# Kernel tuning notes

Measured on AMD Instinct MI355X. Metric: run time of the kernel, lower is better.

Reference implementation:

```python
import jax, jax.numpy as jnp
import numpy as np
from jax import lax

WIN = 7  # hard-coded winsize in PSF.forward
EPS = 1e-8


def _box_sum(x, n):
    # Sliding n x n window sum with zero padding (== ZeroPad2d(n//2) + unfold sum),
    return lax.reduce_window(x, 0.0, lax.add, (1, 1, n, n), (1, 1, 1, 1), 'SAME')


def _patch_stats(x, n):
    n2 = n * n
    s = _box_sum(x, n)
    s2 = _box_sum(x * x, n)
    mean = s / n2
    # torch .var() default is unbiased (divide by N-1)
    var = (s2 - n2 * mean * mean) / (n2 - 1)
    return mean, jnp.maximum(var, 0.0)


def patch_mv_norm(x, n):
    mean, var = _patch_stats(x, n)
    return (x - mean) / (jnp.sqrt(var) + EPS)


def patch_adain(x, y, n):
    x_norm = patch_mv_norm(x, n)
    y_mean, y_var = _patch_stats(y, n)
    return x_norm * jnp.sqrt(y_var) + y_mean  # note: no eps on y_std, as in source


def conv1x1(x, w, b):
    # x: (B,C,H,W), w: (O,C), b: (O,)
    return jnp.einsum('oc,bchw->bohw', w, x) + b[None, :, None, None]


def setup_inputs() -> dict:
    key = jax.random.key(0)
    ks = jax.random.split(key, 12)
    B, C, H, W = 8, 256, 128, 128
    front = jax.random.normal(ks[0], (B, C, H, W), dtype=jnp.float32)
    back = jax.random.normal(ks[1], (B, C, H, W), dtype=jnp.float32)
    mask = jax.random.uniform(ks[2], (B, 1, H, W), dtype=jnp.float32)
    scale = 0.02
    we = jax.random.normal(ks[3], (C, C), dtype=jnp.float32) * scale
    wf = jax.random.normal(ks[4], (C, C), dtype=jnp.float32) * scale
    wg = jax.random.normal(ks[5], (C, C), dtype=jnp.float32) * scale
    wh = jax.random.normal(ks[6], (C, C), dtype=jnp.float32) * scale
    be = jax.random.normal(ks[7], (C,), dtype=jnp.float32) * scale
    bf = jax.random.normal(ks[8], (C,), dtype=jnp.float32) * scale
    bg = jax.random.normal(ks[9], (C,), dtype=jnp.float32) * scale
    bh = jax.random.normal(ks[10], (C,), dtype=jnp.float32) * scale
    return {'front': front, 'back': back, 'mask': mask,
            'we': we, 'be': be, 'wf': wf, 'bf': bf,
            'wg': wg, 'bg': bg, 'wh': wh, 'bh': bh}


def reference(front, back, mask, we, be, wf, bf, wg, bg, wh, bh):
    b, c, h, w = front.shape
    EE = conv1x1(patch_adain(front, back, WIN), we, be)
    FF = conv1x1(patch_mv_norm(front, WIN), wf, bf)
    GG = conv1x1(patch_mv_norm(back, WIN), wg, bg)
    HH = conv1x1(back, wh, bh)
    # channel-wise cosine similarity between FF and GG
    F_n = jnp.sqrt(jnp.sum(FF * FF, axis=1))  # (B,H,W)
    G_n = jnp.sqrt(jnp.sum(GG * GG, axis=1))
    S = jnp.sum(FF * GG, axis=1) / (F_n * G_n)
    # per-sample spatial min-max normalization
    S_flat = S.reshape(b, h * w)
    s_min = jnp.min(S_flat, axis=1, keepdims=True)
    s_max = jnp.max(S_flat, axis=1, keepdims=True)
    S_n = ((S_flat - s_min) / (s_max - s_min)).reshape(b, 1, h, w)
    fused = S_n * EE + (1.0 - S_n) * HH
    return fused
```

## Files before the change

kernel.cpp:

```cpp
#include <hip/hip_runtime.h>
#include <math.h>

#define PIX 16384
#define TSZ ((size_t)33554432)

typedef __attribute__((ext_vector_type(8))) short  short8;
typedef __attribute__((ext_vector_type(4))) float  float4v;
typedef __attribute__((ext_vector_type(4))) unsigned int uint4v;
typedef __attribute__((ext_vector_type(2))) unsigned int uint2v;

__device__ __forceinline__ unsigned short f2bf(float x) {
  unsigned int u = __float_as_uint(x);
  u += 0x7fffu + ((u >> 16) & 1u);
  return (unsigned short)(u >> 16);
}
__device__ __forceinline__ float bf2f(unsigned short h) {
  return __uint_as_float(((unsigned int)h) << 16);
}
__device__ __forceinline__ unsigned int pack_bf2(float lo, float hi) {
  unsigned int ul = __float_as_uint(lo); ul += 0x7fffu + ((ul >> 16) & 1u);
  unsigned int uh = __float_as_uint(hi); uh += 0x7fffu + ((uh >> 16) & 1u);
  return __builtin_amdgcn_perm(uh, ul, 0x07060302u);
}

#define SB0   __builtin_amdgcn_sched_barrier(0)
#define BARR  __builtin_amdgcn_s_barrier()
#define LGKM0 asm volatile("s_waitcnt lgkmcnt(0)" ::: "memory")
#define VMC(n) asm volatile("s_waitcnt vmcnt(" #n ")" ::: "memory")

__global__ __launch_bounds__(256) void k_prep(const float* __restrict__ we,
                                              const float* __restrict__ wf,
                                              const float* __restrict__ wg,
                                              const float* __restrict__ wh,
                                              unsigned short* __restrict__ wbf) {
  int idx = blockIdx.x * 256 + threadIdx.x;
  int g = idx >> 16, within = idx & 65535;
  const float* src = (g == 0) ? wf : (g == 1) ? wg : (g == 2) ? we : wh;
  int e    = within & 7;
  int lane = (within >> 3) & 63;
  int im   = (within >> 9) & 3;
  int wv   = (within >> 11) & 3;
  int i    = within >> 13;
  int col = lane & 15, q = lane >> 4;
  int m = wv * 64 + im * 16 + col;
  int k = i * 32 + q * 8 + e;
  wbf[idx] = f2bf(src[m * 256 + k]);
}

__global__ __launch_bounds__(256, 4) void k_stats(const float* __restrict__ front,
                                                  const float* __restrict__ back,
                                                  unsigned short* __restrict__ xcm) {
  int blk = blockIdx.x;
  int s   = blk & 7;
  int c   = (blk >> 3) & 255;
  int b   = blk >> 11;
  int t   = threadIdx.x;
  int r0  = s * 16;

  __shared__ float2 vspD[16 * 137];

  size_t planeOff = ((size_t)(b * 256 + c)) * PIX;

  float meanR[8], sdR[8];

  #pragma unroll 1
  for (int phase = 0; phase < 2; ++phase) {
    const float* src = (phase == 0 ? back : front) + planeOff;
    {
      int col = t & 127;
      int rg  = (t >> 7) * 8;
      const float* colp = src + col;
      float xv[14];
      #pragma unroll
      for (int j = 0; j < 14; ++j) {
        int g = r0 + rg - 3 + j;
        float v = 0.f;
        if (g >= 0 && g < 128) v = colp[g * 128];
        xv[j] = v;
      }
      float sm = 0.f, s2 = 0.f;
      #pragma unroll
      for (int j = 0; j < 7; ++j) { sm += xv[j]; s2 = fmaf(xv[j], xv[j], s2); }
      vspD[rg * 137 + col + 3] = make_float2(sm, s2);
      #pragma unroll
      for (int o = 1; o < 8; ++o) {
        float vn = xv[o + 6], vo = xv[o - 1];
        sm += vn - vo;
        s2 += vn * vn - vo * vo;
        vspD[(rg + o) * 137 + col + 3] = make_float2(sm, s2);
      }
      if (t < 96) {
        int rr = t & 15;
        int pc = t >> 4;
        int ac = (pc < 3) ? pc : 128 + pc;
        vspD[rr * 137 + ac] = make_float2(0.f, 0.f);
      }
    }
    LGKM0; BARR;
    {
      int r  = t & 15;
      int c0 = (t >> 4) * 8;
      float2 w[14];
      #pragma unroll
      for (int i = 0; i < 14; ++i) w[i] = vspD[r * 137 + c0 + i];
      float4v x0 = *(const float4v*)(src + (r0 + r) * 128 + c0);
      float4v x1 = *(const float4v*)(src + (r0 + r) * 128 + c0 + 4);
      float xc[8] = {x0[0], x0[1], x0[2], x0[3], x1[0], x1[1], x1[2], x1[3]};
      float sm = 0.f, s2 = 0.f;
      #pragma unroll
      for (int i = 0; i < 7; ++i) { sm += w[i].x; s2 += w[i].y; }
      float nrmv[8], hv[8];
      #pragma unroll
      for (int o = 0; o < 8; ++o) {
        float mean = sm * (1.f / 49.f);
        float var  = (s2 - sm * mean) * (1.f / 48.f);
        var = var > 0.f ? var : 0.f;
        float sd = __builtin_amdgcn_sqrtf(var);
        float x  = xc[o];
        float nrm = (x - mean) * __builtin_amdgcn_rcpf(sd + 1e-8f);
        if (phase == 0) { meanR[o] = mean; sdR[o] = sd; hv[o] = x; }
        else            { hv[o] = nrm * sdR[o] + meanR[o]; }
        nrmv[o] = nrm;
        if (o < 7) { sm += w[o + 7].x - w[o].x; s2 += w[o + 7].y - w[o].y; }
      }
      uint4v nv  = (uint4v){pack_bf2(nrmv[0], nrmv[1]), pack_bf2(nrmv[2], nrmv[3]),
                            pack_bf2(nrmv[4], nrmv[5]), pack_bf2(nrmv[6], nrmv[7])};
      uint4v hvv = (uint4v){pack_bf2(hv[0], hv[1]), pack_bf2(hv[2], hv[3]),
                            pack_bf2(hv[4], hv[5]), pack_bf2(hv[6], hv[7])};
      int p = (r0 + r) * 128 + c0;
      size_t gb2 = (((size_t)(b * 256 + (p >> 6))) * 256 + c) * 64 + (p & 63);
      int tn0 = (phase == 0) ? 1 : 0;
      int tn1 = (phase == 0) ? 3 : 2;
      *(uint4v*)(xcm + (size_t)tn0 * TSZ + gb2) = nv;
      *(uint4v*)(xcm + (size_t)tn1 * TSZ + gb2) = hvv;
    }
    LGKM0; BARR;
  }
}

__device__ __forceinline__ void stage_tile(const unsigned short* __restrict__ Xt,
                                           int k0, int t,
                                           unsigned short* dst) {
  int kk = ((t >> 5) << 2) + ((t & 7) >> 1);
  int px = (((t >> 3) & 3) << 4) + ((t & 1) << 3);
  const unsigned short* src = Xt + (size_t)(k0 << 6) + (kk << 6) + px;
  typedef const __attribute__((address_space(1))) unsigned int GUI;
  typedef __attribute__((address_space(3))) unsigned int LUI;
  __builtin_amdgcn_global_load_lds((GUI*)(unsigned long long)src,
                                   (LUI*)(unsigned)(unsigned long long)(dst + t * 8),
                                   16, 0, 0);
}

#define LOADA(S, I) {                                           \
  af[S][0] = *(const short8*)(Wr + (I) * 8192 + 0 * 512);       \
  af[S][1] = *(const short8*)(Wr + (I) * 8192 + 1 * 512);       \
  af[S][2] = *(const short8*)(Wr + (I) * 8192 + 2 * 512);       \
  af[S][3] = *(const short8*)(Wr + (I) * 8192 + 3 * 512); }

#define TR8(O0,O1,O2,O3,O4,O5,O6,O7)                                              \
  asm volatile("ds_read_b64_tr_b16 %0, %1 offset:" #O0 : "=v"(r0) : "v"(tra));    \
  asm volatile("ds_read_b64_tr_b16 %0, %1 offset:" #O1 : "=v"(r1) : "v"(tra));    \
  asm volatile("ds_read_b64_tr_b16 %0, %1 offset:" #O2 : "=v"(r2) : "v"(tra));    \
  asm volatile("ds_read_b64_tr_b16 %0, %1 offset:" #O3 : "=v"(r3) : "v"(tra));    \
  asm volatile("ds_read_b64_tr_b16 %0, %1 offset:" #O4 : "=v"(r4) : "v"(tra));    \
  asm volatile("ds_read_b64_tr_b16 %0, %1 offset:" #O5 : "=v"(r5) : "v"(tra));    \
  asm volatile("ds_read_b64_tr_b16 %0, %1 offset:" #O6 : "=v"(r6) : "v"(tra));    \
  asm volatile("ds_read_b64_tr_b16 %0, %1 offset:" #O7 : "=v"(r7) : "v"(tra));

#define DOMFMA(MS) {                                                        \
  union BU { unsigned u[4]; short8 s; } bu0, bu1, bu2, bu3;                 \
  bu0.u[0]=r0[0]; bu0.u[1]=r0[1]; bu0.u[2]=r1[0]; bu0.u[3]=r1[1];           \
  bu1.u[0]=r2[0]; bu1.u[1]=r2[1]; bu1.u[2]=r3[0]; bu1.u[3]=r3[1];           \
  bu2.u[0]=r4[0]; bu2.u[1]=r4[1]; bu2.u[2]=r5[0]; bu2.u[3]=r5[1];           \
  bu3.u[0]=r6[0]; bu3.u[1]=r6[1]; bu3.u[2]=r7[0]; bu3.u[3]=r7[1];           \
  short8 bv0 = bu0.s, bv1 = bu1.s, bv2 = bu2.s, bv3 = bu3.s;                \
  _Pragma("unroll")                                                         \
  for (int im = 0; im < 4; ++im) {                                          \
    acc[0][im] = __builtin_amdgcn_mfma_f32_16x16x32_bf16(af[MS][im], bv0, acc[0][im], 0, 0, 0); \
    acc[1][im] = __builtin_amdgcn_mfma_f32_16x16x32_bf16(af[MS][im], bv1, acc[1][im], 0, 0, 0); \
    acc[2][im] = __builtin_amdgcn_mfma_f32_16x16x32_bf16(af[MS][im], bv2, acc[2][im], 0, 0, 0); \
    acc[3][im] = __builtin_amdgcn_mfma_f32_16x16x32_bf16(af[MS][im], bv3, acc[3][im], 0, 0, 0); \
  } }

#define GSTEP(VN, DOSTAGE, K0, SLOT, DOA, AS, AI, MS, O0,O1,O2,O3,O4,O5,O6,O7) \
  SB0;                                                                          \
  if (DOSTAGE) stage_tile(X, K0, t, xt + (SLOT) * 2048);                        \
  SB0;                                                                          \
  if (DOA) LOADA(AS, AI);                                                       \
  SB0;                                                                          \
  VMC(VN);                                                                      \
  SB0; BARR; SB0;                                                               \
  TR8(O0,O1,O2,O3,O4,O5,O6,O7);                                                 \
  LGKM0; SB0;                                                                   \
  DOMFMA(MS);

__device__ __forceinline__ void gemm_pipe(const unsigned short* __restrict__ X,
                                          const unsigned short* __restrict__ Wm,
                                          unsigned short* xt, unsigned xbase,
                                          int mbase, int lane, int t,
                                          float4v acc[4][4]) {
  unsigned tra = xbase + (unsigned)((((lane >> 4)) << 10) + ((lane & 15) << 3));
  const unsigned short* __restrict__ Wr = Wm + ((mbase >> 6) << 11) + lane * 8;

  short8 af[2][4];
  uint2v r0, r1, r2, r3, r4, r5, r6, r7;

  #pragma unroll
  for (int in = 0; in < 4; ++in)
    #pragma unroll
    for (int im = 0; im < 4; ++im)
      acc[in][im] = (float4v){0.f, 0.f, 0.f, 0.f};

  SB0; BARR; SB0;
  stage_tile(X,  0, t, xt + 0 * 2048);
  stage_tile(X, 32, t, xt + 1 * 2048);
  stage_tile(X, 64, t, xt + 2 * 2048);
  SB0;
  LOADA(0, 0);
  SB0;

  GSTEP( 5,  1,  96,  3,   1, 1, 1, 0,      0,  512,  128,  640,  256,  768,  384,  896)
  GSTEP( 5,  1, 128,  4,   1, 0, 2, 1,   4096, 4608, 4224, 4736, 4352, 4864, 4480, 4992)
  GSTEP( 5,  1, 160,  0,   1, 1, 3, 0,   8192, 8704, 8320, 8832, 8448, 8960, 8576, 9088)
  GSTEP( 5,  1, 192,  1,   1, 0, 4, 1,  12288,12800,12416,12928,12544,13056,12672,13184)
  GSTEP( 5,  1, 224,  2,   1, 1, 5, 0,  16384,16896,16512,17024,16640,17152,16768,17280)
  GSTEP( 4,  0,   0,  0,   1, 0, 6, 1,      0,  512,  128,  640,  256,  768,  384,  896)
  GSTEP( 4,  0,   0,  0,   1, 1, 7, 0,   4096, 4608, 4224, 4736, 4352, 4864, 4480, 4992)
  GSTEP( 0,  0,   0,  0,   0, 0, 0, 1,   8192, 8704, 8320, 8832, 8448, 8960, 8576, 9088)
}

__global__ __launch_bounds__(256, 3) void k_gemm1(const unsigned short* __restrict__ xcm,
                                                  const unsigned short* __restrict__ wbf,
                                                  const float* __restrict__ bFF,
                                                  const float* __restrict__ bGG,
                                                  float* __restrict__ Sout) {
  int blk  = blockIdx.x;
  int b    = blk >> 8;
  int pt   = blk & 255;
  int p0   = pt * 64;
  int t    = threadIdx.x;
  int wv   = t >> 6;
  int lane = t & 63;
  int q    = lane >> 4;
  int mbase = wv * 64;

  __shared__ __align__(16) unsigned short xt[5][2048];
  __shared__ float sred[3 * 64];
  if (t < 192) sred[t] = 0.f;
  __syncthreads();
  unsigned xbase = (unsigned)(unsigned long long)&xt[0][0];

  const unsigned short* Xt = xcm + (((size_t)(b * 256 + pt)) << 14);

  float4v aF[4][4], aG[4][4];

  gemm_pipe(Xt + 0 * TSZ, wbf + 0 * 65536, &xt[0][0], xbase, mbase, lane, t, aF);
  gemm_pipe(Xt + 1 * TSZ, wbf + 1 * 65536, &xt[0][0], xbase, mbase, lane, t, aG);
  #pragma unroll
  for (int im = 0; im < 4; ++im) {
    float4v bvF = *(const float4v*)(bFF + mbase + im * 16 + q * 4);
    float4v bvG = *(const float4v*)(bGG + mbase + im * 16 + q * 4);
    #pragma unroll
    for (int in = 0; in < 4; ++in) { aF[in][im] += bvF; aG[in][im] += bvG; }
  }
  #pragma unroll
  for (int in = 0; in < 4; ++in) {
    float d = 0.f, nf = 0.f, ng = 0.f;
    #pragma unroll
    for (int im = 0; im < 4; ++im)
      #pragma unroll
      for (int r = 0; r < 4; ++r) {
        float f = aF[in][im][r], g = aG[in][im][r];
        d += f * g; nf += f * f; ng += g * g;
      }
    d  += __shfl_xor(d, 16);  d  += __shfl_xor(d, 32);
    nf += __shfl_xor(nf, 16); nf += __shfl_xor(nf, 32);
    ng += __shfl_xor(ng, 16); ng += __shfl_xor(ng, 32);
    if (lane < 16) {
      atomicAdd(&sred[0 * 64 + in * 16 + lane], d);
      atomicAdd(&sred[1 * 64 + in * 16 + lane], nf);
      atomicAdd(&sred[2 * 64 + in * 16 + lane], ng);
    }
  }
  __syncthreads();
  if (t < 64) {
    float d = sred[t], nf = sred[64 + t], ng = sred[128 + t];
    Sout[(size_t)b * PIX + p0 + t] = d / (sqrtf(nf) * sqrtf(ng));
  }
}

__global__ __launch_bounds__(256, 3) void k_gemm2(const unsigned short* __restrict__ xcm,
                                                  const unsigned short* __restrict__ wbf,
                                                  const float* __restrict__ bEE,
                                                  const float* __restrict__ bHH,
                                                  const float* __restrict__ S,
                                                  const float* __restrict__ mm,
                                                  float* __restrict__ out) {
  int blk  = blockIdx.x;
  int b    = blk >> 8;
  int pt   = blk & 255;
  int p0   = pt * 64;
  int t    = threadIdx.x;
  int wv   = t >> 6;
  int lane = t & 63;
  int col  = lane & 15;
  int q    = lane >> 4;
  int mbase = wv * 64;

  __shared__ __align__(16) unsigned short xt[5][2048];
  unsigned xbase = (unsigned)(unsigned long long)&xt[0][0];

  const unsigned short* Xt = xcm + (((size_t)(b * 256 + pt)) << 14);

  float4v aE[4][4], aH[4][4];

  gemm_pipe(Xt + 2 * TSZ, wbf + 2 * 65536, &xt[0][0], xbase, mbase, lane, t, aE);
  gemm_pipe(Xt + 3 * TSZ, wbf + 3 * 65536, &xt[0][0], xbase, mbase, lane, t, aH);

  float mn = mm[b * 2], mx = mm[b * 2 + 1];
  float inv = 1.f / (mx - mn);
  float sn[4];
  #pragma unroll
  for (int in = 0; in < 4; ++in)
    sn[in] = (S[(size_t)b * PIX + p0 + in * 16 + col] - mn) * inv;

  #pragma unroll
  for (int im = 0; im < 4; ++im) {
    float4v bvE = *(const float4v*)(bEE + mbase + im * 16 + q * 4);
    float4v bvH = *(const float4v*)(bHH + mbase + im * 16 + q * 4);
    #pragma unroll
    for (int in = 0; in < 4; ++in)
      #pragma unroll
      for (int r = 0; r < 4; ++r) {
        int m = mbase + im * 16 + q * 4 + r;
        float e = aE[in][im][r] + bvE[r];
        float h = aH[in][im][r] + bvH[r];
        out[((size_t)(b * 256 + m)) * PIX + p0 + in * 16 + col] = h + sn[in] * (e - h);
      }
  }
}

__global__ __launch_bounds__(256) void k_minmax(const float* __restrict__ S,
                                                float* __restrict__ mm) {
  int b = blockIdx.x, t = threadIdx.x;
  const float* sp = S + (size_t)b * PIX;
  float mn = 3.0e38f, mx = -3.0e38f;
  for (int i = t; i < PIX; i += 256) { float v = sp[i]; mn = fminf(mn, v); mx = fmaxf(mx, v); }
  #pragma unroll
  for (int o = 32; o >= 1; o >>= 1) {
    mn = fminf(mn, __shfl_xor(mn, o));
    mx = fmaxf(mx, __shfl_xor(mx, o));
  }
  __shared__ float smn[4], smx[4];
  if ((t & 63) == 0) { smn[t >> 6] = mn; smx[t >> 6] = mx; }
  __syncthreads();
  if (t == 0) {
    mn = fminf(fminf(smn[0], smn[1]), fminf(smn[2], smn[3]));
    mx = fmaxf(fmaxf(smx[0], smx[1]), fmaxf(smx[2], smx[3]));
    mm[b * 2] = mn; mm[b * 2 + 1] = mx;
  }
}

extern "C" void kernel_launch(void* const* d_in, const int* in_sizes, int n_in,
                              void* d_out, int out_size, void* d_ws, size_t ws_size,
                              hipStream_t stream) {
  const float* front = (const float*)d_in[0];
  const float* back  = (const float*)d_in[1];
  const float* we = (const float*)d_in[3];
  const float* be = (const float*)d_in[4];
  const float* wf = (const float*)d_in[5];
  const float* bf = (const float*)d_in[6];
  const float* wg = (const float*)d_in[7];
  const float* bg = (const float*)d_in[8];
  const float* wh = (const float*)d_in[9];
  const float* bh = (const float*)d_in[10];

  char* ws = (char*)d_ws;
  unsigned short* xcm  = (unsigned short*)(ws);
  unsigned short* wbf  = (unsigned short*)(ws + 268435456);
  float*          S    = (float*)(ws + 268959744);
  float*          mm   = (float*)(ws + 269484032);
  float*          out  = (float*)d_out;

  k_prep  <<<1024,  256, 0, stream>>>(we, wf, wg, wh, wbf);
  k_stats <<<16384, 256, 0, stream>>>(front, back, xcm);
  k_gemm1 <<<2048,  256, 0, stream>>>(xcm, wbf, bf, bg, S);
  k_minmax<<<8,     256, 0, stream>>>(S, mm);
  k_gemm2 <<<2048,  256, 0, stream>>>(xcm, wbf, be, bh, S, mm, out);
}
```

Measured before the change: 542.7 us.

## Interleave paired GEMMs with deep LDS staging and fuse min-max via atomics

The two back-to-back GEMM pipelines in each kernel are merged into one interleaved pipeline that stages larger chunks of both operand tiles into a 64 KB LDS buffer and alternates MFMA work between the two accumulators. The separate min-max kernel is removed; gemm1 instead reduces each tile's similarity and updates per-batch min/max with atomics on order-preserving uint keys, initialised in the prep kernel. The aim is fewer barriers and pipeline prologues plus one fewer launch. In exchange, occupancy drops from 3 to 2 blocks per CU, and the tile-sized atomics add a small cost.

Measured after the change: 517.3 us. 1.05x faster.

```diff
diff --git a/kernel.cpp b/kernel.cpp
--- a/kernel.cpp
+++ b/kernel.cpp
@@ -23,6 +23,15 @@
   return __builtin_amdgcn_perm(uh, ul, 0x07060302u);
 }
 
+__device__ __forceinline__ unsigned int fkey(float f) {
+  unsigned int u = __float_as_uint(f);
+  return (u & 0x80000000u) ? ~u : (u | 0x80000000u);
+}
+__device__ __forceinline__ float funkey(unsigned int k) {
+  unsigned int u = (k & 0x80000000u) ? (k ^ 0x80000000u) : ~k;
+  return __uint_as_float(u);
+}
+
 #define SB0   __builtin_amdgcn_sched_barrier(0)
 #define BARR  __builtin_amdgcn_s_barrier()
 #define LGKM0 asm volatile("s_waitcnt lgkmcnt(0)" ::: "memory")
@@ -32,7 +41,10 @@
                                               const float* __restrict__ wf,
                                               const float* __restrict__ wg,
                                               const float* __restrict__ wh,
-                                              unsigned short* __restrict__ wbf) {
+                                              unsigned short* __restrict__ wbf,
+                                              unsigned int* __restrict__ mmu) {
+  if (blockIdx.x == 0 && threadIdx.x < 16)
+    mmu[threadIdx.x] = (threadIdx.x & 1) ? 0u : 0xFFFFFFFFu;
   int idx = blockIdx.x * 256 + threadIdx.x;
   int g = idx >> 16, within = idx & 65535;
   const float* src = (g == 0) ? wf : (g == 1) ? wg : (g == 2) ? we : wh;
@@ -151,11 +163,11 @@
                                    16, 0, 0);
 }
 
-#define LOADA(S, I) {                                           \
-  af[S][0] = *(const short8*)(Wr + (I) * 8192 + 0 * 512);       \
-  af[S][1] = *(const short8*)(Wr + (I) * 8192 + 1 * 512);       \
-  af[S][2] = *(const short8*)(Wr + (I) * 8192 + 2 * 512);       \
-  af[S][3] = *(const short8*)(Wr + (I) * 8192 + 3 * 512); }
+#define LOADA(WP, S, I) {                                       \
+  af[S][0] = *(const short8*)(WP + (I) * 8192 + 0 * 512);       \
+  af[S][1] = *(const short8*)(WP + (I) * 8192 + 1 * 512);       \
+  af[S][2] = *(const short8*)(WP + (I) * 8192 + 2 * 512);       \
+  af[S][3] = *(const short8*)(WP + (I) * 8192 + 3 * 512); }
 
 #define TR8(O0,O1,O2,O3,O4,O5,O6,O7)                                              \
   asm volatile("ds_read_b64_tr_b16 %0, %1 offset:" #O0 : "=v"(r0) : "v"(tra));    \
@@ -167,7 +179,7 @@
   asm volatile("ds_read_b64_tr_b16 %0, %1 offset:" #O6 : "=v"(r6) : "v"(tra));    \
   asm volatile("ds_read_b64_tr_b16 %0, %1 offset:" #O7 : "=v"(r7) : "v"(tra));
 
-#define DOMFMA(MS) {                                                        \
+#define DOMFMA(ACC, MS) {                                                   \
   union BU { unsigned u[4]; short8 s; } bu0, bu1, bu2, bu3;                 \
   bu0.u[0]=r0[0]; bu0.u[1]=r0[1]; bu0.u[2]=r1[0]; bu0.u[3]=r1[1];           \
   bu1.u[0]=r2[0]; bu1.u[1]=r2[1]; bu1.u[2]=r3[0]; bu1.u[3]=r3[1];           \
@@ -176,31 +188,29 @@
   short8 bv0 = bu0.s, bv1 = bu1.s, bv2 = bu2.s, bv3 = bu3.s;                \
   _Pragma("unroll")                                                         \
   for (int im = 0; im < 4; ++im) {                                          \
-    acc[0][im] = __builtin_amdgcn_mfma_f32_16x16x32_bf16(af[MS][im], bv0, acc[0][im], 0, 0, 0); \
-    acc[1][im] = __builtin_amdgcn_mfma_f32_16x16x32_bf16(af[MS][im], bv1, acc[1][im], 0, 0, 0); \
-    acc[2][im] = __builtin_amdgcn_mfma_f32_16x16x32_bf16(af[MS][im], bv2, acc[2][im], 0, 0, 0); \
-    acc[3][im] = __builtin_amdgcn_mfma_f32_16x16x32_bf16(af[MS][im], bv3, acc[3][im], 0, 0, 0); \
+    ACC[0][im] = __builtin_amdgcn_mfma_f32_16x16x32_bf16(af[MS][im], bv0, ACC[0][im], 0, 0, 0); \
+    ACC[1][im] = __builtin_amdgcn_mfma_f32_16x16x32_bf16(af[MS][im], bv1, ACC[1][im], 0, 0, 0); \
+    ACC[2][im] = __builtin_amdgcn_mfma_f32_16x16x32_bf16(af[MS][im], bv2, ACC[2][im], 0, 0, 0); \
+    ACC[3][im] = __builtin_amdgcn_mfma_f32_16x16x32_bf16(af[MS][im], bv3, ACC[3][im], 0, 0, 0); \
   } }
 
-#define GSTEP(VN, DOSTAGE, K0, SLOT, DOA, AS, AI, MS, O0,O1,O2,O3,O4,O5,O6,O7) \
-  SB0;                                                                          \
-  if (DOSTAGE) stage_tile(X, K0, t, xt + (SLOT) * 2048);                        \
-  SB0;                                                                          \
-  if (DOA) LOADA(AS, AI);                                                       \
-  SB0;                                                                          \
-  VMC(VN);                                                                      \
-  SB0; BARR; SB0;                                                               \
-  TR8(O0,O1,O2,O3,O4,O5,O6,O7);                                                 \
-  LGKM0; SB0;                                                                   \
-  DOMFMA(MS);
-
-__device__ __forceinline__ void gemm_pipe(const unsigned short* __restrict__ X,
-                                          const unsigned short* __restrict__ Wm,
-                                          unsigned short* xt, unsigned xbase,
-                                          int mbase, int lane, int t,
-                                          float4v acc[4][4]) {
+#define FHALF(OA0,OA1,OA2,OA3,OA4,OA5,OA6,OA7, OB0,OB1,OB2,OB3,OB4,OB5,OB6,OB7)   \
+  TR8(OA0,OA1,OA2,OA3,OA4,OA5,OA6,OA7); LGKM0; SB0; DOMFMA(accF, 0);              \
+  TR8(OB0,OB1,OB2,OB3,OB4,OB5,OB6,OB7); LGKM0; SB0; DOMFMA(accF, 1);
+#define GHALF(OA0,OA1,OA2,OA3,OA4,OA5,OA6,OA7, OB0,OB1,OB2,OB3,OB4,OB5,OB6,OB7)   \
+  TR8(OA0,OA1,OA2,OA3,OA4,OA5,OA6,OA7); LGKM0; SB0; DOMFMA(accG, 0);              \
+  TR8(OB0,OB1,OB2,OB3,OB4,OB5,OB6,OB7); LGKM0; SB0; DOMFMA(accG, 1);
+
+__device__ __forceinline__ void gemm_pipe2(const unsigned short* __restrict__ X1,
+                                           const unsigned short* __restrict__ X2,
+                                           const unsigned short* __restrict__ Wm1,
+                                           const unsigned short* __restrict__ Wm2,
+                                           unsigned short* xt, unsigned xbase,
+                                           int mbase, int lane, int t,
+                                           float4v accF[4][4], float4v accG[4][4]) {
   unsigned tra = xbase + (unsigned)((((lane >> 4)) << 10) + ((lane & 15) << 3));
-  const unsigned short* __restrict__ Wr = Wm + ((mbase >> 6) << 11) + lane * 8;
+  const unsigned short* __restrict__ Wr1 = Wm1 + ((mbase >> 6) << 11) + lane * 8;
+  const unsigned short* __restrict__ Wr2 = Wm2 + ((mbase >> 6) << 11) + lane * 8;
 
   short8 af[2][4];
   uint2v r0, r1, r2, r3, r4, r5, r6, r7;
@@ -208,32 +218,73 @@
   #pragma unroll
   for (int in = 0; in < 4; ++in)
     #pragma unroll
-    for (int im = 0; im < 4; ++im)
-      acc[in][im] = (float4v){0.f, 0.f, 0.f, 0.f};
+    for (int im = 0; im < 4; ++im) {
+      accF[in][im] = (float4v){0.f, 0.f, 0.f, 0.f};
+      accG[in][im] = (float4v){0.f, 0.f, 0.f, 0.f};
+    }
 
   SB0; BARR; SB0;
-  stage_tile(X,  0, t, xt + 0 * 2048);
-  stage_tile(X, 32, t, xt + 1 * 2048);
-  stage_tile(X, 64, t, xt + 2 * 2048);
+  stage_tile(X1,   0, t, xt + 0 * 2048);
+  stage_tile(X1,  32, t, xt + 1 * 2048);
+  stage_tile(X1,  64, t, xt + 2 * 2048);
+  stage_tile(X1,  96, t, xt + 3 * 2048);
+  stage_tile(X2,   0, t, xt + 8 * 2048);
+  stage_tile(X2,  32, t, xt + 9 * 2048);
+  stage_tile(X2,  64, t, xt + 10 * 2048);
+  stage_tile(X2,  96, t, xt + 11 * 2048);
   SB0;
-  LOADA(0, 0);
-  SB0;
-
-  GSTEP( 5,  1,  96,  3,   1, 1, 1, 0,      0,  512,  128,  640,  256,  768,  384,  896)
-  GSTEP( 5,  1, 128,  4,   1, 0, 2, 1,   4096, 4608, 4224, 4736, 4352, 4864, 4480, 4992)
-  GSTEP( 5,  1, 160,  0,   1, 1, 3, 0,   8192, 8704, 8320, 8832, 8448, 8960, 8576, 9088)
-  GSTEP( 5,  1, 192,  1,   1, 0, 4, 1,  12288,12800,12416,12928,12544,13056,12672,13184)
-  GSTEP( 5,  1, 224,  2,   1, 1, 5, 0,  16384,16896,16512,17024,16640,17152,16768,17280)
-  GSTEP( 4,  0,   0,  0,   1, 0, 6, 1,      0,  512,  128,  640,  256,  768,  384,  896)
-  GSTEP( 4,  0,   0,  0,   1, 1, 7, 0,   4096, 4608, 4224, 4736, 4352, 4864, 4480, 4992)
-  GSTEP( 0,  0,   0,  0,   0, 0, 0, 1,   8192, 8704, 8320, 8832, 8448, 8960, 8576, 9088)
-}
-
-__global__ __launch_bounds__(256, 3) void k_gemm1(const unsigned short* __restrict__ xcm,
+
+  LOADA(Wr1, 0, 0); LOADA(Wr1, 1, 1); SB0;
+  VMC(0); SB0; BARR; SB0;
+  FHALF(    0,   512,   128,   640,   256,   768,   384,   896,
+         4096,  4608,  4224,  4736,  4352,  4864,  4480,  4992)
+  SB0; LOADA(Wr2, 0, 0); LOADA(Wr2, 1, 1); SB0;
+  stage_tile(X1, 128, t, xt + 4 * 2048);
+  stage_tile(X1, 160, t, xt + 5 * 2048);
+  stage_tile(X2, 128, t, xt + 12 * 2048);
+  stage_tile(X2, 160, t, xt + 13 * 2048);
+  SB0; VMC(4); SB0;
+  GHALF(32768, 33280, 32896, 33408, 33024, 33536, 33152, 33664,
+        36864, 37376, 36992, 37504, 37120, 37632, 37248, 37760)
+
+  SB0; LOADA(Wr1, 0, 2); LOADA(Wr1, 1, 3); SB0;
+  VMC(0); SB0; BARR; SB0;
+  FHALF( 8192,  8704,  8320,  8832,  8448,  8960,  8576,  9088,
+        12288, 12800, 12416, 12928, 12544, 13056, 12672, 13184)
+  SB0; LOADA(Wr2, 0, 2); LOADA(Wr2, 1, 3); SB0;
+  stage_tile(X1, 192, t, xt + 6 * 2048);
+  stage_tile(X1, 224, t, xt + 7 * 2048);
+  stage_tile(X2, 192, t, xt + 14 * 2048);
+  stage_tile(X2, 224, t, xt + 15 * 2048);
+  SB0; VMC(4); SB0;
+  GHALF(40960, 41472, 41088, 41600, 41216, 41728, 41344, 41856,
+        45056, 45568, 45184, 45696, 45312, 45824, 45440, 45952)
+
+  SB0; LOADA(Wr1, 0, 4); LOADA(Wr1, 1, 5); SB0;
+  VMC(0); SB0; BARR; SB0;
+  FHALF(16384, 16896, 16512, 17024, 16640, 17152, 16768, 17280,
+        20480, 20992, 20608, 21120, 20736, 21248, 20864, 21376)
+  SB0; LOADA(Wr2, 0, 4); LOADA(Wr2, 1, 5); SB0;
+  VMC(0); SB0;
+  GHALF(49152, 49664, 49280, 49792, 49408, 49920, 49536, 50048,
+        53248, 53760, 53376, 53888, 53504, 54016, 53632, 54144)
+
+  SB0; LOADA(Wr1, 0, 6); LOADA(Wr1, 1, 7); SB0;
+  VMC(0); SB0; BARR; SB0;
+  FHALF(24576, 25088, 24704, 25216, 24832, 25344, 24960, 25472,
+        28672, 29184, 28800, 29312, 28928, 29440, 29056, 29568)
+  SB0; LOADA(Wr2, 0, 6); LOADA(Wr2, 1, 7); SB0;
+  VMC(0); SB0;
+  GHALF(57344, 57856, 57472, 57984, 57600, 58112, 57728, 58240,
+        61440, 61952, 61568, 62080, 61696, 62208, 61824, 62336)
+}
+
+__global__ __launch_bounds__(256, 2) void k_gemm1(const unsigned short* __restrict__ xcm,
                                                   const unsigned short* __restrict__ wbf,
                                                   const float* __restrict__ bFF,
                                                   const float* __restrict__ bGG,
-                                                  float* __restrict__ Sout) {
+                                                  float* __restrict__ Sout,
+                                                  unsigned int* __restrict__ mmu) {
   int blk  = blockIdx.x;
   int b    = blk >> 8;
   int pt   = blk & 255;
@@ -244,7 +295,7 @@
   int q    = lane >> 4;
   int mbase = wv * 64;
 
-  __shared__ __align__(16) unsigned short xt[5][2048];
+  __shared__ __align__(16) unsigned short xt[16][2048];
   __shared__ float sred[3 * 64];
   if (t < 192) sred[t] = 0.f;
   __syncthreads();
@@ -253,9 +304,9 @@
   const unsigned short* Xt = xcm + (((size_t)(b * 256 + pt)) << 14);
 
   float4v aF[4][4], aG[4][4];
-
-  gemm_pipe(Xt + 0 * TSZ, wbf + 0 * 65536, &xt[0][0], xbase, mbase, lane, t, aF);
-  gemm_pipe(Xt + 1 * TSZ, wbf + 1 * 65536, &xt[0][0], xbase, mbase, lane, t, aG);
+  gemm_pipe2(Xt + 0 * TSZ, Xt + 1 * TSZ, wbf + 0 * 65536, wbf + 1 * 65536,
+             &xt[0][0], xbase, mbase, lane, t, aF, aG);
+
   #pragma unroll
   for (int im = 0; im < 4; ++im) {
     float4v bvF = *(const float4v*)(bFF + mbase + im * 16 + q * 4);
@@ -285,16 +336,27 @@
   __syncthreads();
   if (t < 64) {
     float d = sred[t], nf = sred[64 + t], ng = sred[128 + t];
-    Sout[(size_t)b * PIX + p0 + t] = d / (sqrtf(nf) * sqrtf(ng));
+    float sv = d / (sqrtf(nf) * sqrtf(ng));
+    Sout[(size_t)b * PIX + p0 + t] = sv;
+    float mn = sv, mx = sv;
+    #pragma unroll
+    for (int o = 32; o >= 1; o >>= 1) {
+      mn = fminf(mn, __shfl_xor(mn, o));
+      mx = fmaxf(mx, __shfl_xor(mx, o));
+    }
+    if (t == 0) {
+      atomicMin(&mmu[b * 2],     fkey(mn));
+      atomicMax(&mmu[b * 2 + 1], fkey(mx));
+    }
   }
 }
 
-__global__ __launch_bounds__(256, 3) void k_gemm2(const unsigned short* __restrict__ xcm,
+__global__ __launch_bounds__(256, 2) void k_gemm2(const unsigned short* __restrict__ xcm,
                                                   const unsigned short* __restrict__ wbf,
                                                   const float* __restrict__ bEE,
                                                   const float* __restrict__ bHH,
                                                   const float* __restrict__ S,
-                                                  const float* __restrict__ mm,
+                                                  const unsigned int* __restrict__ mmu,
                                                   float* __restrict__ out) {
   int blk  = blockIdx.x;
   int b    = blk >> 8;
@@ -307,17 +369,16 @@
   int q    = lane >> 4;
   int mbase = wv * 64;
 
-  __shared__ __align__(16) unsigned short xt[5][2048];
+  __shared__ __align__(16) unsigned short xt[16][2048];
   unsigned xbase = (unsigned)(unsigned long long)&xt[0][0];
 
   const unsigned short* Xt = xcm + (((size_t)(b * 256 + pt)) << 14);
 
   float4v aE[4][4], aH[4][4];
-
-  gemm_pipe(Xt + 2 * TSZ, wbf + 2 * 65536, &xt[0][0], xbase, mbase, lane, t, aE);
-  gemm_pipe(Xt + 3 * TSZ, wbf + 3 * 65536, &xt[0][0], xbase, mbase, lane, t, aH);
-
-  float mn = mm[b * 2], mx = mm[b * 2 + 1];
+  gemm_pipe2(Xt + 2 * TSZ, Xt + 3 * TSZ, wbf + 2 * 65536, wbf + 3 * 65536,
+             &xt[0][0], xbase, mbase, lane, t, aE, aH);
+
+  float mn = funkey(mmu[b * 2]), mx = funkey(mmu[b * 2 + 1]);
   float inv = 1.f / (mx - mn);
   float sn[4];
   #pragma unroll
@@ -337,27 +398,6 @@
         float h = aH[in][im][r] + bvH[r];
         out[((size_t)(b * 256 + m)) * PIX + p0 + in * 16 + col] = h + sn[in] * (e - h);
       }
-  }
-}
-
-__global__ __launch_bounds__(256) void k_minmax(const float* __restrict__ S,
-                                                float* __restrict__ mm) {
-  int b = blockIdx.x, t = threadIdx.x;
-  const float* sp = S + (size_t)b * PIX;
-  float mn = 3.0e38f, mx = -3.0e38f;
-  for (int i = t; i < PIX; i += 256) { float v = sp[i]; mn = fminf(mn, v); mx = fmaxf(mx, v); }
-  #pragma unroll
-  for (int o = 32; o >= 1; o >>= 1) {
-    mn = fminf(mn, __shfl_xor(mn, o));
-    mx = fmaxf(mx, __shfl_xor(mx, o));
-  }
-  __shared__ float smn[4], smx[4];
-  if ((t & 63) == 0) { smn[t >> 6] = mn; smx[t >> 6] = mx; }
-  __syncthreads();
-  if (t == 0) {
-    mn = fminf(fminf(smn[0], smn[1]), fminf(smn[2], smn[3]));
-    mx = fmaxf(fmaxf(smx[0], smx[1]), fmaxf(smx[2], smx[3]));
-    mm[b * 2] = mn; mm[b * 2 + 1] = mx;
   }
 }
 
@@ -379,12 +419,11 @@
   unsigned short* xcm  = (unsigned short*)(ws);
   unsigned short* wbf  = (unsigned short*)(ws + 268435456);
   float*          S    = (float*)(ws + 268959744);
-  float*          mm   = (float*)(ws + 269484032);
+  unsigned int*   mmu  = (unsigned int*)(ws + 269484032);
   float*          out  = (float*)d_out;
 
-  k_prep  <<<1024,  256, 0, stream>>>(we, wf, wg, wh, wbf);
+  k_prep  <<<1024,  256, 0, stream>>>(we, wf, wg, wh, wbf, mmu);
   k_stats <<<16384, 256, 0, stream>>>(front, back, xcm);
-  k_gemm1 <<<2048,  256, 0, stream>>>(xcm, wbf, bf, bg, S);
-  k_minmax<<<8,     256, 0, stream>>>(S, mm);
-  k_gemm2 <<<2048,  256, 0, stream>>>(xcm, wbf, be, bh, S, mm, out);
-}
+  k_gemm1 <<<2048,  256, 0, stream>>>(xcm, wbf, bf, bg, S, mmu);
+  k_gemm2 <<<2048,  256, 0, stream>>>(xcm, wbf, be, bh, S, mmu, out);
+}
```
